# Performance work log

Hardware: AMD Instinct MI355X
Metric: run time of the kernel (lower is better)

## Reference

```python
import jax, jax.numpy as jnp
import numpy as np

B, T = 128, 50
VOCAB, EMB_D, GRU_H = 10000, 200, 100
HEADS, AHID, THID = 8, 96, 96

def _conv(x, w, b, pad):
    y = jax.lax.conv_general_dilated(x, w, (1, 1), pad,
        dimension_numbers=('NCHW', 'OIHW', 'NCHW'))
    return y + b[None, :, None, None]

def _bn(x, g, b, m, v):
    s = jax.lax.rsqrt(v + 1e-5)
    return (x - m[None, :, None, None]) * (g * s)[None, :, None, None] + b[None, :, None, None]

def _maxpool(x):
    return jax.lax.reduce_window(x, -jnp.inf, jax.lax.max, (1, 1, 2, 2), (1, 1, 2, 2), 'VALID')

def _resize(x):
    # F.interpolate(mode='bilinear', align_corners=False) == half-pixel bilinear, no antialias
    return jax.image.resize(x, (x.shape[0], x.shape[1], 25, 156), 'bilinear', antialias=False)

def _audio_attn(x, wq, bq, wk, bk, wv, bv):
    # x: [B,96,H,W]; wq: [heads,96,96] == stacked per-head 1x1 convs
    Q = jnp.einsum('bchw,noc->bnohw', x, wq) + bq[None, :, :, None, None]
    K = jnp.einsum('bchw,noc->bnohw', x, wk) + bk[None, :, :, None, None]
    V = jnp.einsum('bchw,noc->bnohw', x, wv) + bv[None, :, :, None, None]
    # torch F.softmax with no dim on a 4D tensor defaults to dim=1 (channels) -> axis=2 here
    return jax.nn.softmax(Q * K, axis=2) * V  # [B,heads,96,H,W]

def _text_attn(o, wq, bq, wk, bk, wv, bv):
    # o: [N,100]; wq: [heads,96,100] == stacked per-head Linear layers
    Q = jnp.einsum('nd,hod->nho', o, wq) + bq[None]
    K = jnp.einsum('nd,hod->nho', o, wk) + bk[None]
    V = jnp.einsum('nd,hod->nho', o, wv) + bv[None]
    a = jax.nn.softmax(Q * K, axis=2) * V  # 2D softmax default dim=1 -> over feature axis
    return a.reshape(o.shape[0], -1)  # head-concat order == torch cat along dim=1

def _gru(xs, w_ih, w_hh, b_ih, b_hh):
    # xs: [T,B,200]; torch gate order r, z, n; b_hn applied inside r-gating
    def step(h, x):
        gi = x @ w_ih.T + b_ih
        gh = h @ w_hh.T + b_hh
        ir, iz, inew = jnp.split(gi, 3, axis=1)
        hr, hz, hnew = jnp.split(gh, 3, axis=1)
        r = jax.nn.sigmoid(ir + hr)
        z = jax.nn.sigmoid(iz + hz)
        n = jnp.tanh(inew + r * hnew)
        h2 = (1.0 - z) * n + z * h
        return h2, h2
    h0 = jnp.zeros((xs.shape[1], GRU_H), xs.dtype)
    hT, outs = jax.lax.scan(step, h0, xs)
    return outs, hT

def _forward(tokens, lengths, mfcc_t, mfcc_f, mfcc_c, w1a, b1a, g1a, be1a, m1a, v1a, w1b, b1b, g1b, be1b, m1b, v1b, w2, b2, g2, be2, m2, v2, w3, b3, g3, be3, m3, v3, w4, b4, g4, be4, m4, v4, wq_a1, bq_a1, wk_a1, bk_a1, wv_a1, bv_a1, wq_a2, bq_a2, wk_a2, bk_a2, wv_a2, bv_a2, emb, w_ih, w_hh, b_ih, b_hh, wq_t1, bq_t1, wk_t1, bk_t1, wv_t1, bv_t1, wq_t2, bq_t2, wk_t2, bk_t2, wv_t2, bv_t2, w_fa, b_fa, w_ft, b_ft, w_e, b_e):
    # --- audio CNN stem (eval-mode batchnorm; dropout off) ---
    xa = jax.nn.relu(_bn(_conv(mfcc_t, w1a, b1a, 'VALID'), g1a, be1a, m1a, v1a))
    xb = jax.nn.relu(_bn(_conv(mfcc_f, w1b, b1b, 'VALID'), g1b, be1b, m1b, v1b))
    # NOTE: original source reuses conv1b/bn1b for the third input (faithful to that)
    xc = jax.nn.relu(_bn(_conv(mfcc_c, w1b, b1b, 'VALID'), g1b, be1b, m1b, v1b))
    x = jnp.concatenate([_resize(xa), _resize(xb), _resize(xc)], axis=1)  # [B,24,25,156]
    x = _maxpool(jax.nn.relu(_bn(_conv(x, w2, b2, [(1, 1), (1, 1)]), g2, be2, m2, v2)))  # [B,32,12,78]
    x = _maxpool(jax.nn.relu(_bn(_conv(x, w3, b3, [(1, 1), (1, 1)]), g3, be3, m3, v3)))  # [B,64,6,39]
    x = jax.nn.relu(_bn(_conv(x, w4, b4, [(1, 1), (1, 1)]), g4, be4, m4, v4))            # [B,96,6,39]
    # --- two stacked per-head audio attentions, then per-head spatial GAP ---
    a1 = _audio_attn(x, wq_a1, bq_a1, wk_a1, bk_a1, wv_a1, bv_a1).mean(axis=(-2, -1))  # [B,8,96]
    a2 = _audio_attn(x, wq_a2, bq_a2, wk_a2, bk_a2, wv_a2, bv_a2).mean(axis=(-2, -1))
    # forward() slices heads along the height concat and GAPs -> per head [stage1 96, stage2 96]
    self_attn_audio = jnp.concatenate([a1, a2], axis=2).reshape(x.shape[0], -1)  # [B,1536]
    # --- text branch: embedding + GRU (all lengths == T -> pack/pad is identity) ---
    ex = jnp.swapaxes(emb[tokens], 0, 1)  # [T,B,200]
    outs, h = _gru(ex, w_ih, w_hh, b_ih, b_hh)  # h: [B,100]
    output = jnp.swapaxes(outs, 0, 1).reshape(-1, GRU_H)  # [B*T,100]
    t1 = _text_attn(output, wq_t1, bq_t1, wk_t1, bk_t1, wv_t1, bv_t1)
    t2 = _text_attn(output, wq_t2, bq_t2, wk_t2, bk_t2, wv_t2, bv_t2)
    self_attn_text = jnp.concatenate([t1, t2], axis=1).reshape(x.shape[0], T, -1).sum(axis=1)  # [B,1536]
    # --- cross-modal gated fusion ---
    x_gap = x.mean(axis=(-2, -1))  # [B,96]
    a_text = jax.nn.softmax(x_gap @ w_fa.T + b_fa, axis=1)   # [B,100]
    attn_text_based_audio = a_text * h                        # [B,100]
    a_audio = jax.nn.softmax(h @ w_ft.T + b_ft, axis=1)      # [B,96]
    attn_audio_based_text = a_audio * x_gap                   # [B,96]
    feat = jnp.concatenate([self_attn_audio, self_attn_text,
                            attn_audio_based_text, attn_text_based_audio], axis=1)  # [B,3268]
    return feat @ w_e.T + b_e  # [B,4] emotion logits

def setup_inputs() -> dict:
    key = jax.random.key(0)
    ks = iter(jax.random.split(key, 100))
    nrm = lambda s, sc=0.05: jax.random.normal(next(ks), s, jnp.float32) * sc
    uni = lambda s: jax.random.uniform(next(ks), s, jnp.float32) * 0.5 + 0.5
    d = {}
    d['mfcc_t'] = jax.random.normal(next(ks), (B, 1, 200, 40), jnp.float32)
    d['mfcc_f'] = jax.random.normal(next(ks), (B, 1, 200, 40), jnp.float32)
    d['mfcc_c'] = jax.random.normal(next(ks), (B, 1, 200, 40), jnp.float32)
    d['tokens'] = jax.random.randint(next(ks), (B, T), 0, VOCAB)
    d['lengths'] = jnp.full((B,), T, jnp.int32)
    def bnp(pre, c):
        d['g' + pre] = 1.0 + nrm((c,)); d['be' + pre] = nrm((c,))
        d['m' + pre] = nrm((c,)); d['v' + pre] = uni((c,))
    d['w1a'] = nrm((8, 1, 5, 2), 0.2); d['b1a'] = nrm((8,)); bnp('1a', 8)
    d['w1b'] = nrm((8, 1, 2, 6), 0.2); d['b1b'] = nrm((8,)); bnp('1b', 8)
    d['w2'] = nrm((32, 24, 3, 3), 0.1); d['b2'] = nrm((32,)); bnp('2', 32)
    d['w3'] = nrm((64, 32, 3, 3), 0.1); d['b3'] = nrm((64,)); bnp('3', 64)
    d['w4'] = nrm((96, 64, 3, 3), 0.08); d['b4'] = nrm((96,)); bnp('4', 96)
    for s in ('1', '2'):
        for p in ('q', 'k', 'v'):
            d['w%s_a%s' % (p, s)] = nrm((HEADS, 96, 96), 0.1)
            d['b%s_a%s' % (p, s)] = nrm((HEADS, 96))
    d['emb'] = nrm((VOCAB, EMB_D), 0.1)
    d['w_ih'] = nrm((3 * GRU_H, EMB_D), 0.1); d['w_hh'] = nrm((3 * GRU_H, GRU_H), 0.1)
    d['b_ih'] = nrm((3 * GRU_H,)); d['b_hh'] = nrm((3 * GRU_H,))
    for s in ('1', '2'):
        for p in ('q', 'k', 'v'):
            d['w%s_t%s' % (p, s)] = nrm((HEADS, THID, GRU_H), 0.1)
            d['b%s_t%s' % (p, s)] = nrm((HEADS, THID))
    d['w_fa'] = nrm((100, 96), 0.1); d['b_fa'] = nrm((100,))
    d['w_ft'] = nrm((96, 100), 0.1); d['b_ft'] = nrm((96,))
    d['w_e'] = nrm((4, 2 * HEADS * AHID + 2 * HEADS * THID + 96 + 100), 0.05); d['b_e'] = nrm((4,))
    return d

def reference(mfcc_t, mfcc_f, mfcc_c, tokens, lengths, w1a, b1a, g1a, be1a, m1a, v1a, w1b, b1b, g1b, be1b, m1b, v1b, w2, b2, g2, be2, m2, v2, w3, b3, g3, be3, m3, v3, w4, b4, g4, be4, m4, v4, wq_a1, bq_a1, wk_a1, bk_a1, wv_a1, bv_a1, wq_a2, bq_a2, wk_a2, bk_a2, wv_a2, bv_a2, emb, w_ih, w_hh, b_ih, b_hh, wq_t1, bq_t1, wk_t1, bk_t1, wv_t1, bv_t1, wq_t2, bq_t2, wk_t2, bk_t2, wv_t2, bv_t2, w_fa, b_fa, w_ft, b_ft, w_e, b_e):
    return _forward(tokens, lengths, mfcc_t, mfcc_f, mfcc_c, w1a, b1a, g1a, be1a, m1a, v1a, w1b, b1b, g1b, be1b, m1b, v1b, w2, b2, g2, be2, m2, v2, w3, b3, g3, be3, m3, v3, w4, b4, g4, be4, m4, v4, wq_a1, bq_a1, wk_a1, bk_a1, wv_a1, bv_a1, wq_a2, bq_a2, wk_a2, bk_a2, wv_a2, bv_a2, emb, w_ih, w_hh, b_ih, b_hh, wq_t1, bq_t1, wk_t1, bk_t1, wv_t1, bv_t1, wq_t2, bq_t2, wk_t2, bk_t2, wv_t2, bv_t2, w_fa, b_fa, w_ft, b_ft, w_e, b_e)
```

## Files before the change

### kernel.cpp

```cpp
#include <hip/hip_runtime.h>
#include <math.h>

static constexpr int kB = 128;
static constexpr int kT = 50;

struct TDesc { const float* src; float* dst; int O; int C; int total; };
struct TPack { TDesc d[15]; };
__global__ void k_transpose_pack(TPack p, float* __restrict__ za) {
    if (blockIdx.y == 15) {
        for (int i = blockIdx.x * 256 + threadIdx.x; i < 196608; i += 76800)
            za[i] = 0.f;
        return;
    }
    TDesc t = p.d[blockIdx.y];
    int idx = blockIdx.x * 256 + threadIdx.x;
    if (idx >= t.total) return;
    int o = idx % t.O; int r = idx / t.O; int c = r % t.C; int n = r / t.C;
    t.dst[idx] = t.src[((size_t)n * t.O + o) * t.C + c];
}

__global__ void __launch_bounds__(320) k_gi(const int* __restrict__ tokens,
        const float* __restrict__ emb, const float* __restrict__ w_ih,
        const float* __restrict__ b_ih, float* __restrict__ GI) {
    int r0 = blockIdx.x * 8;
// ... 18 lines not shown
            }
        }
        #pragma unroll
        for (int r = 0; r < 8; ++r)
            GI[(size_t)(r0 + r) * 300 + tid] = acc[r];
    }
}

__global__ void __launch_bounds__(256) k_fat_stem_gru(
    const float* __restrict__ mt, const float* __restrict__ mf,
    const float* __restrict__ mc,
    const float* __restrict__ w1a, const float* __restrict__ b1a,
    const float* __restrict__ g1a, const float* __restrict__ be1a,
    const float* __restrict__ m1a, const float* __restrict__ v1a,
    const float* __restrict__ w1b, const float* __restrict__ b1b,
    const float* __restrict__ g1b, const float* __restrict__ be1b,
    const float* __restrict__ m1b, const float* __restrict__ v1b,
    float* __restrict__ out, int total,
    const float* __restrict__ GI, const float* __restrict__ w_hh,
    const float* __restrict__ b_hh, float* __restrict__ outsT) {
    if (blockIdx.x < 128) {
        const int b = blockIdx.x, tid = threadIdx.x;
        __shared__ float hs[100];
        __shared__ float gH[300];
        const float bias0 = b_hh[tid];
        const float bias1 = (tid < 44) ? b_hh[256 + tid] : 0.f;
        if (tid < 100) hs[tid] = 0.f;
        __syncthreads();
        for (int t = 0; t < kT; ++t) {
            {
                float gh = bias0;
                const float* wr = w_hh + (size_t)tid * 100;
                #pragma unroll
                for (int k4 = 0; k4 < 25; ++k4) {
                    float4 w4 = *(const float4*)(wr + k4 * 4);
                    float4 h4 = *(const float4*)&hs[k4 * 4];
                    gh += w4.x * h4.x + w4.y * h4.y + w4.z * h4.z + w4.w * h4.w;
                }
                gH[tid] = gh;
            }
            if (tid < 44) {
                float gh = bias1;
                const float* wr = w_hh + (size_t)(256 + tid) * 100;
                #pragma unroll
                for (int k4 = 0; k4 < 25; ++k4) {
                    float4 w4 = *(const float4*)(wr + k4 * 4);
                    float4 h4 = *(const float4*)&hs[k4 * 4];
                    gh += w4.x * h4.x + w4.y * h4.y + w4.z * h4.z + w4.w * h4.w;
                }
                gH[256 + tid] = gh;
            }
            __syncthreads();
            if (tid < 100) {
                const float* gi = GI + ((size_t)b * kT + t) * 300;
                float r = 1.f / (1.f + expf(-(gi[tid] + gH[tid])));
                float z = 1.f / (1.f + expf(-(gi[100 + tid] + gH[100 + tid])));
                float nn = tanhf(gi[200 + tid] + r * gH[200 + tid]);
                float h2 = (1.f - z) * nn + z * hs[tid];
                hs[tid] = h2;
                outsT[((size_t)b * 100 + tid) * kT + t] = h2;
            }
            __syncthreads();
        }
        return;
    }
    int idx = (blockIdx.x - 128) * 256 + threadIdx.x;
    if (idx >= total) return;
    int ox = idx % 156; int t = idx / 156;
    int oy = t % 25; t /= 25;
    int grp = t % 3; int b = t / 3;
    const float* src; int Hc, Wc;
    const float *wb0, *cb, *g, *be, *m, *v;
    if (grp == 0) { src = mt; Hc = 196; Wc = 39; wb0 = w1a;
                    cb = b1a; g = g1a; be = be1a; m = m1a; v = v1a; }
    else          { src = (grp == 1 ? mf : mc); Hc = 199; Wc = 35; wb0 = w1b;
                    cb = b1b; g = g1b; be = be1b; m = m1b; v = v1b; }
    float sy = (oy + 0.5f) * ((float)Hc / 25.f) - 0.5f;
    float sx = (ox + 0.5f) * ((float)Wc / 156.f) - 0.5f;
    float fy0 = floorf(sy), fx0 = floorf(sx);
    float fy = sy - fy0, fx = sx - fx0;
    int y0 = (int)fy0, x0 = (int)fx0;
    int y0c = min(max(y0, 0), Hc - 1), y1c = min(max(y0 + 1, 0), Hc - 1);
    int x0c = min(max(x0, 0), Wc - 1), x1c = min(max(x0 + 1, 0), Wc - 1);
    bool xs = (x1c == x0c), ys = (y1c == y0c);
    const float* p = src + (size_t)b * 8000;
    float* ob_ = out + (((size_t)b * 24 + grp * 8) * 25 + oy) * 156 + ox;
    const float w00 = (1.f - fy) * (1.f - fx), w01 = (1.f - fy) * fx;
    const float w10 = fy * (1.f - fx),         w11 = fy * fx;
    if (grp == 0) {
        float W[6][3];
        #pragma unroll
        for (int r = 0; r < 6; ++r) {
            int rr = min(y0c + r, 199);
            #pragma unroll
            for (int cc = 0; cc < 3; ++cc)
                W[r][cc] = p[rr * 40 + min(x0c + cc, 39)];
        }
        #pragma unroll
        for (int c = 0; c < 8; ++c) {
            const float* wb = wb0 + c * 10;
            float a00 = 0.f, a01 = 0.f, a10 = 0.f, a11 = 0.f;
            #pragma unroll
            for (int ky = 0; ky < 5; ++ky)
                #pragma unroll
                for (int kx = 0; kx < 2; ++kx) {
                    float wv = wb[ky * 2 + kx];
                    a00 += W[ky][kx] * wv;     a01 += W[ky][kx + 1] * wv;
                    a10 += W[ky + 1][kx] * wv; a11 += W[ky + 1][kx + 1] * wv;
                }
            float t00 = a00;
            float t01 = xs ? a00 : a01;
            float t10 = ys ? a00 : a10;
            float t11 = xs ? (ys ? a00 : a10) : (ys ? a01 : a11);
            float s = g[c] * rsqrtf(v[c] + 1e-5f);
            float bias = (cb[c] - m[c]) * s + be[c];
            float r00 = fmaxf(t00 * s + bias, 0.f), r01 = fmaxf(t01 * s + bias, 0.f);
            float r10 = fmaxf(t10 * s + bias, 0.f), r11 = fmaxf(t11 * s + bias, 0.f);
            ob_[c * 3900] = r00 * w00 + r01 * w01 + r10 * w10 + r11 * w11;
        }
    } else {
        float W[3][7];
        #pragma unroll
        for (int r = 0; r < 3; ++r) {
            int rr = min(y0c + r, 199);
            #pragma unroll
            for (int cc = 0; cc < 7; ++cc)
                W[r][cc] = p[rr * 40 + min(x0c + cc, 39)];
        }
        #pragma unroll
        for (int c = 0; c < 8; ++c) {
            const float* wb = wb0 + c * 12;
            float a00 = 0.f, a01 = 0.f, a10 = 0.f, a11 = 0.f;
            #pragma unroll
            for (int ky = 0; ky < 2; ++ky)
                #pragma unroll
                for (int kx = 0; kx < 6; ++kx) {
                    float wv = wb[ky * 6 + kx];
                    a00 += W[ky][kx] * wv;     a01 += W[ky][kx + 1] * wv;
                    a10 += W[ky + 1][kx] * wv; a11 += W[ky + 1][kx + 1] * wv;
                }
            float t00 = a00;
            float t01 = xs ? a00 : a01;
            float t10 = ys ? a00 : a10;
            float t11 = xs ? (ys ? a00 : a10) : (ys ? a01 : a11);
            float s = g[c] * rsqrtf(v[c] + 1e-5f);
            float bias = (cb[c] - m[c]) * s + be[c];
            float r00 = fmaxf(t00 * s + bias, 0.f), r01 = fmaxf(t01 * s + bias, 0.f);
            float r10 = fmaxf(t10 * s + bias, 0.f), r11 = fmaxf(t11 * s + bias, 0.f);
            ob_[c * 3900] = r00 * w00 + r01 * w01 + r10 * w10 + r11 * w11;
        }
    }
}

template<int CIN, int CI_T, int H, int W, int ROWS, int NPX, bool POOL>
__global__ void __launch_bounds__(256) k_conv16(
    const float* __restrict__ in, const float* __restrict__ wT,
    const float* __restrict__ cb, const float* __restrict__ g,
    const float* __restrict__ be, const float* __restrict__ m,
    const float* __restrict__ v, float* __restrict__ out, int COUT, int PHT) {
    constexpr int WP = W + 2;
    constexpr int RP = ROWS + 2;
    constexpr int STAGE = CI_T * RP * WP;
    __shared__ float sx[STAGE];
    __shared__ float sw[CI_T * 9 * 16];
    const int b = blockIdx.x, rt = blockIdx.y, oc0 = blockIdx.z * 16;
    const int row0 = rt * ROWS;
    const int tid = threadIdx.x;

    int off[NPX]; bool val[NPX];
    #pragma unroll
    for (int j = 0; j < NPX; ++j) {
        int px = tid + j * 256;
        int oy = px / W, ox = px - oy * W;
        bool ok = (px < ROWS * W) && (row0 + oy < H);
        val[j] = ok;
        off[j] = ok ? (oy * WP + ox) : 0;
    }

    float acc[NPX][16];
    #pragma unroll
    for (int j = 0; j < NPX; ++j)
        #pragma unroll
        for (int o = 0; o < 16; ++o) acc[j][o] = 0.f;

    for (int c0 = 0; c0 < CIN; c0 += CI_T) {
        __syncthreads();
        for (int e = tid; e < STAGE; e += 256) {
            int ci = e / (RP * WP);
            int rem = e - ci * RP * WP;
            int r = rem / WP;
            int xx = rem - r * WP;
            int iy = row0 - 1 + r;
            int ix = xx - 1;
            float vv = 0.f;
            if (iy >= 0 && iy < H && ix >= 0 && ix < W)
                vv = in[((size_t)(b * CIN + c0 + ci) * H + iy) * W + ix];
            sx[e] = vv;
        }
        for (int e = tid; e < CI_T * 9 * 16; e += 256) {
            int rk = e >> 4;
            int o = e & 15;
            sw[e] = wT[((size_t)c0 * 9 + rk) * COUT + oc0 + o];
        }
        __syncthreads();
        #pragma unroll 1
        for (int cl = 0; cl < CI_T; ++cl) {
            const float* sxc = sx + cl * RP * WP;
            #pragma unroll
            for (int k = 0; k < 9; ++k) {
                const int ky = k / 3, kx = k % 3;
                const float* wb_ = sw + (cl * 9 + k) * 16;
                const float4 wa = *(const float4*)(wb_);
                const float4 wb2 = *(const float4*)(wb_ + 4);
                const float4 wc = *(const float4*)(wb_ + 8);
                const float4 wd = *(const float4*)(wb_ + 12);
                #pragma unroll
                for (int j = 0; j < NPX; ++j) {
                    float xv = sxc[off[j] + ky * WP + kx];
                    acc[j][0]  += xv * wa.x;  acc[j][1]  += xv * wa.y;
                    acc[j][2]  += xv * wa.z;  acc[j][3]  += xv * wa.w;
                    acc[j][4]  += xv * wb2.x; acc[j][5]  += xv * wb2.y;
                    acc[j][6]  += xv * wb2.z; acc[j][7]  += xv * wb2.w;
                    acc[j][8]  += xv * wc.x;  acc[j][9]  += xv * wc.y;
                    acc[j][10] += xv * wc.z;  acc[j][11] += xv * wc.w;
                    acc[j][12] += xv * wd.x;  acc[j][13] += xv * wd.y;
                    acc[j][14] += xv * wd.z;  acc[j][15] += xv * wd.w;
                }
            }
        }
    }
    float sc[16], bi[16];
    #pragma unroll
    for (int o = 0; o < 16; ++o) {
        float s = g[oc0 + o] * rsqrtf(v[oc0 + o] + 1e-5f);
        sc[o] = s; bi[o] = (cb[oc0 + o] - m[oc0 + o]) * s + be[oc0 + o];
    }
    if (!POOL) {
        #pragma unroll
        for (int j = 0; j < NPX; ++j) if (val[j]) {
            int px = tid + j * 256;
            int oy = row0 + px / W, ox = px % W;
            #pragma unroll
            for (int o = 0; o < 16; ++o)
                out[((size_t)(b * COUT + oc0 + o) * H + oy) * W + ox] =
                    fmaxf(acc[j][o] * sc[o] + bi[o], 0.f);
        }
    } else {
        constexpr int PH = ROWS / 2, PW = W / 2, PT = PH * PW;
        const int prow0 = rt * PH;
        for (int o = 0; o < 16; ++o) {
            __syncthreads();
            #pragma unroll
            for (int j = 0; j < NPX; ++j) if (val[j]) {
                int px = tid + j * 256;
                sx[px] = fmaxf(acc[j][o] * sc[o] + bi[o], 0.f);
            }
            __syncthreads();
            for (int e = tid; e < PT; e += 256) {
                int py = e / PW, pxl = e - py * PW;
                const float* r0 = sx + (2 * py) * W + 2 * pxl;
                float mv = fmaxf(fmaxf(r0[0], r0[1]), fmaxf(r0[W], r0[W + 1]));
                out[((size_t)(b * COUT + oc0 + o) * PHT + prow0 + py) * PW + pxl] = mv;
            }
        }
    }
}

__global__ void __launch_bounds__(256, 2) k_fat_attn(
    const float* __restrict__ x,
    const float* __restrict__ wq1, const float* __restrict__ bq1,
    const float* __restrict__ wk1, const float* __restrict__ bk1,
    const float* __restrict__ wv1, const float* __restrict__ bv1,
    const float* __restrict__ wq2, const float* __restrict__ bq2,
    const float* __restrict__ wk2, const float* __restrict__ bk2,
    const float* __restrict__ wv2, const float* __restrict__ bv2,
    float* __restrict__ afeat,
    const float* __restrict__ outsT,
    const float* __restrict__ wqt1, const float* __restrict__ bqt1,
    const float* __restrict__ wkt1, const float* __restrict__ bkt1,
    const float* __restrict__ wvt1, const float* __restrict__ bvt1,
    const float* __restrict__ wqt2, const float* __restrict__ bqt2,
    const float* __restrict__ wkt2, const float* __restrict__ bkt2,
    const float* __restrict__ wvt2, const float* __restrict__ bvt2,
    float* __restrict__ tfeat, float* __restrict__ xgap) {
    __shared__ float smem[7040];
    const int bx = blockIdx.x;
    const int tid = threadIdx.x;

    if (bx >= 6144) {
        int b = bx - 6144;
        int wave = tid >> 6, lane = tid & 63;
        for (int c = wave; c < 96; c += 4) {
            const float* row = x + ((size_t)b * 96 + c) * 234;
            float s = 0.f;
            for (int p = lane; p < 234; p += 64) s += row[p];
            #pragma unroll
            for (int off = 1; off < 64; off <<= 1) s += __shfl_xor(s, off);
            if (lane == 0) xgap[b * 96 + c] = s * (1.f / 234.f);
        }
        return;
    }
    if (bx >= 4096) {
        int a = bx - 4096;
        const int b = a & 127;
        int rem = a >> 7;
        const int stage = rem & 1, n = rem >> 1;
        const float* wq = (stage ? wqt2 : wqt1) + n * 9600;
        const float* wk = (stage ? wkt2 : wkt1) + n * 9600;
        const float* wv = (stage ? wvt2 : wvt1) + n * 9600;
        const float* bqn = (stage ? bqt2 : bqt1) + n * 96;
        const float* bkn = (stage ? bkt2 : bkt1) + n * 96;
        const float* bvn = (stage ? bvt2 : bvt1) + n * 96;
        const int to = tid >> 4, tpg = tid & 15;
        const int ob = to * 6;
        const int tA = tpg * 4;
        float* sxc = smem;
        float* sw = smem + 1280;
        float* sred = sw;
        const float* xb = outsT + (size_t)b * (100 * kT);

        float qa[6][4], ka[6][4], va[6][4];
        #pragma unroll
        for (int j = 0; j < 6; ++j) {
            float bq_ = bqn[ob + j], bk_ = bkn[ob + j], bv_ = bvn[ob + j];
            #pragma unroll
            for (int i = 0; i < 4; ++i) { qa[j][i] = bq_; ka[j][i] = bk_; va[j][i] = bv_; }
        }
        for (int c0 = 0; c0 < 100; c0 += 20) {
            __syncthreads();
            for (int e = tid; e < 1280; e += 256) {
                int r = e >> 6, tt = e & 63;
                sxc[e] = (tt < kT) ? xb[(c0 + r) * kT + tt] : 0.f;
            }
            for (int e4 = tid; e4 < 1440; e4 += 256) {
                int mat = (e4 >= 960) ? 2 : (e4 >= 480 ? 1 : 0);
                int r4 = e4 - mat * 480;
                const float* wsrc = (mat == 0) ? wq : (mat == 1 ? wk : wv);
                *(float4*)(sw + mat * 1920 + r4 * 4) = *(const float4*)(wsrc + c0 * 96 + r4 * 4);
            }
            __syncthreads();
            #pragma unroll 4
            for (int cc = 0; cc < 20; ++cc) {
                float4 xa = *(const float4*)(sxc + cc * 64 + tA);
                const float* wr = sw + cc * 96 + ob;
                float2 q01 = *(const float2*)(wr);
                float2 q23 = *(const float2*)(wr + 2);
                float2 q45 = *(const float2*)(wr + 4);
                float2 k01 = *(const float2*)(wr + 1920);
                float2 k23 = *(const float2*)(wr + 1922);
                float2 k45 = *(const float2*)(wr + 1924);
                float2 v01 = *(const float2*)(wr + 3840);
                float2 v23 = *(const float2*)(wr + 3842);
                float2 v45 = *(const float2*)(wr + 3844);
                float wqv[6] = {q01.x, q01.y, q23.x, q23.y, q45.x, q45.y};
                float wkv[6] = {k01.x, k01.y, k23.x, k23.y, k45.x, k45.y};
                float wvv[6] = {v01.x, v01.y, v23.x, v23.y, v45.x, v45.y};
                #pragma unroll
                for (int j = 0; j < 6; ++j) {
                    qa[j][0] += wqv[j] * xa.x; qa[j][1] += wqv[j] * xa.y;
                    qa[j][2] += wqv[j] * xa.z; qa[j][3] += wqv[j] * xa.w;
                    ka[j][0] += wkv[j] * xa.x; ka[j][1] += wkv[j] * xa.y;
                    ka[j][2] += wkv[j] * xa.z; ka[j][3] += wkv[j] * xa.w;
                    va[j][0] += wvv[j] * xa.x; va[j][1] += wvv[j] * xa.y;
                    va[j][2] += wvv[j] * xa.z; va[j][3] += wvv[j] * xa.w;
                }
            }
        }
        float pmx[4] = {-1e30f, -1e30f, -1e30f, -1e30f};
        #pragma unroll
        for (int j = 0; j < 6; ++j)
            #pragma unroll
            for (int i = 0; i < 4; ++i) {
                float sv = qa[j][i] * ka[j][i];
                qa[j][i] = sv;
                pmx[i] = fmaxf(pmx[i], sv);
            }
        __syncthreads();
        #pragma unroll
        for (int i = 0; i < 4; ++i) sred[to * 64 + tA + i] = pmx[i];
        __syncthreads();
        float m_[4];
        #pragma unroll
        for (int i = 0; i < 4; ++i) {
            float mm = -1e30f;
            for (int t = 0; t < 16; ++t) mm = fmaxf(mm, sred[t * 64 + tA + i]);
            m_[i] = mm;
        }
        __syncthreads();
        float z[4] = {0.f, 0.f, 0.f, 0.f};
        #pragma unroll
        for (int j = 0; j < 6; ++j)
            #pragma unroll
            for (int i = 0; i < 4; ++i) {
                float e = __expf(qa[j][i] - m_[i]);
                qa[j][i] = e;
                z[i] += e;
            }
        #pragma unroll
        for (int i = 0; i < 4; ++i) sred[to * 64 + tA + i] = z[i];
        __syncthreads();
        float rz[4];
        #pragma unroll
        for (int i = 0; i < 4; ++i) {
            float zs = 0.f;
            for (int t = 0; t < 16; ++t) zs += sred[t * 64 + tA + i];
            rz[i] = (tA + i < kT) ? 1.f / zs : 0.f;
        }
        __syncthreads();
        #pragma unroll
        for (int j = 0; j < 6; ++j) {
            float po = qa[j][0] * rz[0] * va[j][0]
                     + qa[j][1] * rz[1] * va[j][1]
                     + qa[j][2] * rz[2] * va[j][2]
                     + qa[j][3] * rz[3] * va[j][3];
            sred[(ob + j) * 16 + tpg] = po;
        }
        __syncthreads();
        if (tid < 96) {
            float ssum = 0.f;
            #pragma unroll
            for (int t = 0; t < 16; ++t) ssum += sred[tid * 16 + t];
            tfeat[b * 1536 + stage * 768 + n * 96 + tid] = ssum;
        }
        return;
    }

    const int a = bx;
    const int xp = a & 255;
    const int b = xp >> 1, pt = xp & 1;
    const int n = (a >> 8) & 7, stage = a >> 11;
    const float* wq = (stage ? wq2 : wq1) + n * 9216;
    const float* wk = (stage ? wk2 : wk1) + n * 9216;
    const float* wv = (stage ? wv2 : wv1) + n * 9216;
    const float* bqn = (stage ? bq2 : bq1) + n * 96;
    const float* bkn = (stage ? bk2 : bk1) + n * 96;
    const float* bvn = (stage ? bv2 : bv1) + n * 96;
    const int to = tid >> 4, tpg = tid & 15;
    const int ob = to * 6;
    const int pA = tpg * 4;
    const int p0 = pt * 128;

    float* sxc = smem;
    float* sw = smem + 2048;
    float* sred = sw;

    const float* xb = x + (size_t)b * (96 * 234) + p0;

    float qa[6][8], ka[6][8], va[6][8];
    #pragma unroll
    for (int j = 0; j < 6; ++j) {
        float bq_ = bqn[ob + j], bk_ = bkn[ob + j], bv_ = bvn[ob + j];
        #pragma unroll
        for (int i = 0; i < 8; ++i) { qa[j][i] = bq_; ka[j][i] = bk_; va[j][i] = bv_; }
    }

    for (int c0 = 0; c0 < 96; c0 += 16) {
        __syncthreads();
        {
            #pragma unroll
            for (int it = 0; it < 4; ++it) {
                int e2 = tid + it * 256;
                int r = e2 >> 6, c2 = (e2 & 63) * 2;
                float2 v = make_float2(0.f, 0.f);
                if (p0 + c2 < 234) v = *(const float2*)(xb + (c0 + r) * 234 + c2);
                *(float2*)(sxc + r * 128 + c2) = v;
            }
        }
        for (int e4 = tid; e4 < 1152; e4 += 256) {
            int mat = (e4 >= 768) ? 2 : (e4 >= 384 ? 1 : 0);
            int r4 = e4 - mat * 384;
            const float* wsrc = (mat == 0) ? wq : (mat == 1 ? wk : wv);
            *(float4*)(sw + mat * 1536 + r4 * 4) = *(const float4*)(wsrc + c0 * 96 + r4 * 4);
        }
        __syncthreads();
        #pragma unroll 2
        for (int cc = 0; cc < 16; ++cc) {
            float4 xa = *(const float4*)(sxc + cc * 128 + pA);
            float4 xc = *(const float4*)(sxc + cc * 128 + 64 + pA);
            const float* wr = sw + cc * 96 + ob;
            float2 q01 = *(const float2*)(wr);
            float2 q23 = *(const float2*)(wr + 2);
            float2 q45 = *(const float2*)(wr + 4);
            float2 k01 = *(const float2*)(wr + 1536);
            float2 k23 = *(const float2*)(wr + 1538);
            float2 k45 = *(const float2*)(wr + 1540);
            float2 v01 = *(const float2*)(wr + 3072);
            float2 v23 = *(const float2*)(wr + 3074);
            float2 v45 = *(const float2*)(wr + 3076);
            float wqv[6] = {q01.x, q01.y, q23.x, q23.y, q45.x, q45.y};
            float wkv[6] = {k01.x, k01.y, k23.x, k23.y, k45.x, k45.y};
            float wvv[6] = {v01.x, v01.y, v23.x, v23.y, v45.x, v45.y};
            #pragma unroll
            for (int j = 0; j < 6; ++j) {
                qa[j][0] += wqv[j] * xa.x; qa[j][1] += wqv[j] * xa.y;
                qa[j][2] += wqv[j] * xa.z; qa[j][3] += wqv[j] * xa.w;
                qa[j][4] += wqv[j] * xc.x; qa[j][5] += wqv[j] * xc.y;
                qa[j][6] += wqv[j] * xc.z; qa[j][7] += wqv[j] * xc.w;
                ka[j][0] += wkv[j] * xa.x; ka[j][1] += wkv[j] * xa.y;
                ka[j][2] += wkv[j] * xa.z; ka[j][3] += wkv[j] * xa.w;
                ka[j][4] += wkv[j] * xc.x; ka[j][5] += wkv[j] * xc.y;
                ka[j][6] += wkv[j] * xc.z; ka[j][7] += wkv[j] * xc.w;
                va[j][0] += wvv[j] * xa.x; va[j][1] += wvv[j] * xa.y;
                va[j][2] += wvv[j] * xa.z; va[j][3] += wvv[j] * xa.w;
                va[j][4] += wvv[j] * xc.x; va[j][5] += wvv[j] * xc.y;
                va[j][6] += wvv[j] * xc.z; va[j][7] += wvv[j] * xc.w;
            }
        }
    }

    int col[8];
    #pragma unroll
    for (int i = 0; i < 4; ++i) { col[i] = pA + i; col[4 + i] = 64 + pA + i; }

    float pmx[8];
    #pragma unroll
    for (int i = 0; i < 8; ++i) pmx[i] = -1e30f;
    #pragma unroll
    for (int j = 0; j < 6; ++j)
        #pragma unroll
        for (int i = 0; i < 8; ++i) {
            float sv = qa[j][i] * ka[j][i];
            qa[j][i] = sv;
            pmx[i] = fmaxf(pmx[i], sv);
        }
    __syncthreads();
    #pragma unroll
    for (int i = 0; i < 8; ++i) sred[to * 128 + col[i]] = pmx[i];
    __syncthreads();
    float m_[8];
    #pragma unroll
    for (int i = 0; i < 8; ++i) {
        float mm = -1e30f;
        for (int t = 0; t < 16; ++t) mm = fmaxf(mm, sred[t * 128 + col[i]]);
        m_[i] = mm;
    }
    __syncthreads();
    float z[8];
    #pragma unroll
    for (int i = 0; i < 8; ++i) z[i] = 0.f;
    #pragma unroll
    for (int j = 0; j < 6; ++j)
        #pragma unroll
        for (int i = 0; i < 8; ++i) {
            float e = __expf(qa[j][i] - m_[i]);
            qa[j][i] = e;
            z[i] += e;
        }
    #pragma unroll
    for (int i = 0; i < 8; ++i) sred[to * 128 + col[i]] = z[i];
    __syncthreads();
    float rz[8];
    #pragma unroll
    for (int i = 0; i < 8; ++i) {
        float zs = 0.f;
        for (int t = 0; t < 16; ++t) zs += sred[t * 128 + col[i]];
        rz[i] = (p0 + col[i] < 234) ? 1.f / zs : 0.f;
    }
    __syncthreads();
    #pragma unroll
    for (int j = 0; j < 6; ++j) {
        float po = 0.f;
        #pragma unroll
        for (int i = 0; i < 8; ++i) po += qa[j][i] * rz[i] * va[j][i];
        sred[(ob + j) * 16 + tpg] = po;
    }
    __syncthreads();
    if (tid < 96) {
        float ssum = 0.f;
        #pragma unroll
        for (int t = 0; t < 16; ++t) ssum += sred[tid * 16 + t];
        atomicAdd(afeat + b * 1536 + n * 192 + stage * 96 + tid, ssum * (1.f / 234.f));
    }
}

__global__ void __launch_bounds__(128) k_final(const float* __restrict__ xgap,
    const float* __restrict__ outsT, const float* __restrict__ afeat,
    const float* __restrict__ tfeat,
    const float* __restrict__ w_fa, const float* __restrict__ b_fa,
    const float* __restrict__ w_ft, const float* __restrict__ b_ft,
    const float* __restrict__ w_e, const float* __restrict__ b_e,
    float* __restrict__ out) {
    int b = blockIdx.x; int tid = threadIdx.x;
    __shared__ float xg[96], hv[100], st[100], sa[96], aat[96], atba[100];
    __shared__ float redm[2], reds[2];
    if (tid < 96) xg[tid] = xgap[b * 96 + tid];
    if (tid < 100) hv[tid] = outsT[((size_t)b * 100 + tid) * kT + (kT - 1)];
    __syncthreads();
    if (tid < 100) {
        float acc = b_fa[tid];
        const float* wr = w_fa + tid * 96;
        for (int c = 0; c < 96; ++c) acc += wr[c] * xg[c];
        st[tid] = acc;
    }
    if (tid < 96) {
        float acc = b_ft[tid];
        const float* wr = w_ft + tid * 100;
        for (int c = 0; c < 100; ++c) acc += wr[c] * hv[c];
        sa[tid] = acc;
    }
    __syncthreads();
    if (tid == 0) {
        float mxv = -1e30f; for (int i = 0; i < 100; ++i) mxv = fmaxf(mxv, st[i]);
        float s = 0.f; for (int i = 0; i < 100; ++i) s += expf(st[i] - mxv);
        redm[0] = mxv; reds[0] = s;
    }
    if (tid == 1) {
        float mxv = -1e30f; for (int i = 0; i < 96; ++i) mxv = fmaxf(mxv, sa[i]);
        float s = 0.f; for (int i = 0; i < 96; ++i) s += expf(sa[i] - mxv);
        redm[1] = mxv; reds[1] = s;
    }
    __syncthreads();
    if (tid < 100) atba[tid] = expf(st[tid] - redm[0]) / reds[0] * hv[tid];
    if (tid < 96)  aat[tid]  = expf(sa[tid] - redm[1]) / reds[1] * xg[tid];
    __syncthreads();
    float a0 = 0.f, a1 = 0.f, a2 = 0.f, a3 = 0.f;
    for (int col = tid; col < 3268; col += 128) {
        float f;
        if (col < 1536)      f = afeat[b * 1536 + col];
        else if (col < 3072) f = tfeat[b * 1536 + col - 1536];
        else if (col < 3168) f = aat[col - 3072];
        else                 f = atba[col - 3168];
        a0 += w_e[col] * f;            a1 += w_e[3268 + col] * f;
        a2 += w_e[2 * 3268 + col] * f; a3 += w_e[3 * 3268 + col] * f;
    }
    __shared__ float r4[4][128];
    r4[0][tid] = a0; r4[1][tid] = a1; r4[2][tid] = a2; r4[3][tid] = a3;
    __syncthreads();
    if (tid < 4) {
        float s = 0.f;
        for (int i = 0; i < 128; ++i) s += r4[tid][i];
        out[b * 4 + tid] = s + b_e[tid];
    }
}

extern "C" void kernel_launch(void* const* d_in, const int* in_sizes, int n_in,
                              void* d_out, int out_size, void* d_ws, size_t ws_size,
                              hipStream_t stream) {
    (void)in_sizes; (void)n_in; (void)out_size; (void)ws_size;
    const float* mfcc_t = (const float*)d_in[0];
    const float* mfcc_f = (const float*)d_in[1];
    const float* mfcc_c = (const float*)d_in[2];
    const int*   tokens = (const int*)d_in[3];
    const float *w1a = (const float*)d_in[5],  *b1a = (const float*)d_in[6],
                *g1a = (const float*)d_in[7],  *be1a = (const float*)d_in[8],
                *m1a = (const float*)d_in[9],  *v1a = (const float*)d_in[10];
    const float *w1b = (const float*)d_in[11], *b1b = (const float*)d_in[12],
                *g1b = (const float*)d_in[13], *be1b = (const float*)d_in[14],
                *m1b = (const float*)d_in[15], *v1b = (const float*)d_in[16];
    const float *w2 = (const float*)d_in[17], *b2 = (const float*)d_in[18],
                *g2 = (const float*)d_in[19], *be2 = (const float*)d_in[20],
                *m2 = (const float*)d_in[21], *v2 = (const float*)d_in[22];
    const float *w3 = (const float*)d_in[23], *b3 = (const float*)d_in[24],
                *g3 = (const float*)d_in[25], *be3 = (const float*)d_in[26],
                *m3 = (const float*)d_in[27], *v3 = (const float*)d_in[28];
    const float *w4 = (const float*)d_in[29], *b4 = (const float*)d_in[30],
                *g4 = (const float*)d_in[31], *be4 = (const float*)d_in[32],
                *m4 = (const float*)d_in[33], *v4 = (const float*)d_in[34];
    const float *wq_a1 = (const float*)d_in[35], *bq_a1 = (const float*)d_in[36],
                *wk_a1 = (const float*)d_in[37], *bk_a1 = (const float*)d_in[38],
                *wv_a1 = (const float*)d_in[39], *bv_a1 = (const float*)d_in[40];
    const float *wq_a2 = (const float*)d_in[41], *bq_a2 = (const float*)d_in[42],
                *wk_a2 = (const float*)d_in[43], *bk_a2 = (const float*)d_in[44],
                *wv_a2 = (const float*)d_in[45], *bv_a2 = (const float*)d_in[46];
    const float *emb  = (const float*)d_in[47];
    const float *w_ih = (const float*)d_in[48], *w_hh = (const float*)d_in[49],
                *b_ih = (const float*)d_in[50], *b_hh = (const float*)d_in[51];
    const float *wq_t1 = (const float*)d_in[52], *bq_t1 = (const float*)d_in[53],
                *wk_t1 = (const float*)d_in[54], *bk_t1 = (const float*)d_in[55],
                *wv_t1 = (const float*)d_in[56], *bv_t1 = (const float*)d_in[57];
    const float *wq_t2 = (const float*)d_in[58], *bq_t2 = (const float*)d_in[59],
                *wk_t2 = (const float*)d_in[60], *bk_t2 = (const float*)d_in[61],
                *wv_t2 = (const float*)d_in[62], *bv_t2 = (const float*)d_in[63];
    const float *w_fa = (const float*)d_in[64], *b_fa = (const float*)d_in[65],
                *w_ft = (const float*)d_in[66], *b_ft = (const float*)d_in[67],
                *w_e  = (const float*)d_in[68], *b_e  = (const float*)d_in[69];

    float* ws = (float*)d_ws;
    const size_t Z0 = 0;
    const size_t Z1 = 22091776ull;
    const size_t OUTS  = 34072576ull;
    const size_t AFEAT = 34712576ull;
    const size_t TFEAT = 34909184ull;
    const size_t XGAP  = 35105792ull;
    const size_t WT    = 35118080ull;
    float* GI = ws + Z0;
    float* X1 = ws + Z1;
    float* P2 = ws + Z0;
    float* P3 = ws + Z1;
    float* X4 = ws + Z0;
    float* outsT = ws + OUTS;
    float* afeat = ws + AFEAT;
    float* tfeat = ws + TFEAT;
    float* xgap  = ws + XGAP;
    float* wqa1t = ws + WT;
    float* wka1t = wqa1t + 73728; float* wva1t = wka1t + 73728;
    float* wqa2t = wva1t + 73728; float* wka2t = wqa2t + 73728; float* wva2t = wka2t + 73728;
    float* wqt1t = wva2t + 73728;
    float* wkt1t = wqt1t + 76800; float* wvt1t = wkt1t + 76800;
    float* wqt2t = wvt1t + 76800; float* wkt2t = wqt2t + 76800; float* wvt2t = wkt2t + 76800;
    float* wT2 = tfeat;
    float* wT3 = tfeat + 6912;
    float* wT4 = tfeat + 25344;

    TPack tp;
    tp.d[0]  = {wq_a1, wqa1t, 96, 96, 73728};
    tp.d[1]  = {wk_a1, wka1t, 96, 96, 73728};
    tp.d[2]  = {wv_a1, wva1t, 96, 96, 73728};
    tp.d[3]  = {wq_a2, wqa2t, 96, 96, 73728};
    tp.d[4]  = {wk_a2, wka2t, 96, 96, 73728};
    tp.d[5]  = {wv_a2, wva2t, 96, 96, 73728};
    tp.d[6]  = {w2, wT2, 32, 216, 6912};
    tp.d[7]  = {w3, wT3, 64, 288, 18432};
    tp.d[8]  = {w4, wT4, 96, 576, 55296};
    tp.d[9]  = {wq_t1, wqt1t, 96, 100, 76800};
    tp.d[10] = {wk_t1, wkt1t, 96, 100, 76800};
    tp.d[11] = {wv_t1, wvt1t, 96, 100, 76800};
    tp.d[12] = {wq_t2, wqt2t, 96, 100, 76800};
    tp.d[13] = {wk_t2, wkt2t, 96, 100, 76800};
    tp.d[14] = {wv_t2, wvt2t, 96, 100, 76800};
    k_transpose_pack<<<dim3(300, 16), 256, 0, stream>>>(tp, afeat);

    k_gi<<<kB * kT / 8, 320, 0, stream>>>(tokens, emb, w_ih, b_ih, GI);

    k_fat_stem_gru<<<5978, 256, 0, stream>>>(mfcc_t, mfcc_f, mfcc_c,
        w1a, b1a, g1a, be1a, m1a, v1a,
        w1b, b1b, g1b, be1b, m1b, v1b, X1, 1497600,
        GI, w_hh, b_hh, outsT);

    k_conv16<24, 8, 25, 156, 8, 5, true><<<dim3(128, 3, 2), 256, 0, stream>>>(
        X1, wT2, b2, g2, be2, m2, v2, P2, 32, 12);
    k_conv16<32, 8, 12, 78, 12, 4, true><<<dim3(128, 1, 4), 256, 0, stream>>>(
        P2, wT3, b3, g3, be3, m3, v3, P3, 64, 6);
    k_conv16<64, 16, 6, 39, 6, 1, false><<<dim3(128, 1, 6), 256, 0, stream>>>(
        P3, wT4, b4, g4, be4, m4, v4, X4, 96, 0);

    k_fat_attn<<<6272, 256, 0, stream>>>(X4,
        wqa1t, bq_a1, wka1t, bk_a1, wva1t, bv_a1,
        wqa2t, bq_a2, wka2t, bk_a2, wva2t, bv_a2, afeat,
        outsT,
        wqt1t, bq_t1, wkt1t, bk_t1, wvt1t, bv_t1,
        wqt2t, bq_t2, wkt2t, bk_t2, wvt2t, bv_t2, tfeat, xgap);

    k_final<<<kB, 128, 0, stream>>>(xgap, outsT, afeat, tfeat,
                                    w_fa, b_fa, w_ft, b_ft, w_e, b_e, (float*)d_out);
}
```

Before: 1.281 ms.

## Co-schedule text attention blocks alongside conv2/conv3/conv4 launches

Moves the 2048 text-attention blocks out of the big attention kernel and distributes them across the three conv kernels (1024, 512, 512 extra blocks). Text attention depends only on the GRU output, so it can fill idle CUs while the small conv grids run. The conv weight transposes are moved to a separate workspace region so they no longer alias tfeat, which is now written during the conv stage. The risk is extra shared memory per fused kernel and uneven block mixes hurting occupancy.

```diff
diff --git a/kernel.cpp b/kernel.cpp
--- a/kernel.cpp
+++ b/kernel.cpp
@@ -194,8 +194,140 @@
     }
 }
 
-template<int CIN, int CI_T, int H, int W, int ROWS, int NPX, bool POOL>
-__global__ void __launch_bounds__(256) k_conv16(
+__device__ __forceinline__ void text_attn_block(int a, float* smem,
+    const float* __restrict__ outsT,
+    const float* __restrict__ wqt1, const float* __restrict__ bqt1,
+    const float* __restrict__ wkt1, const float* __restrict__ bkt1,
+    const float* __restrict__ wvt1, const float* __restrict__ bvt1,
+    const float* __restrict__ wqt2, const float* __restrict__ bqt2,
+    const float* __restrict__ wkt2, const float* __restrict__ bkt2,
+    const float* __restrict__ wvt2, const float* __restrict__ bvt2,
+    float* __restrict__ tfeat) {
+    const int tid = threadIdx.x;
+    const int b = a & 127;
+    int rem = a >> 7;
+    const int stage = rem & 1, n = rem >> 1;
+    const float* wq = (stage ? wqt2 : wqt1) + n * 9600;
+    const float* wk = (stage ? wkt2 : wkt1) + n * 9600;
+    const float* wv = (stage ? wvt2 : wvt1) + n * 9600;
+    const float* bqn = (stage ? bqt2 : bqt1) + n * 96;
+    const float* bkn = (stage ? bkt2 : bkt1) + n * 96;
+    const float* bvn = (stage ? bvt2 : bvt1) + n * 96;
+    const int to = tid >> 4, tpg = tid & 15;
+    const int ob = to * 6;
+    const int tA = tpg * 4;
+    float* sxc = smem;
+    float* sw = smem + 1280;
+    float* sred = sw;
+    const float* xb = outsT + (size_t)b * (100 * kT);
+
+    float qa[6][4], ka[6][4], va[6][4];
+    #pragma unroll
+    for (int j = 0; j < 6; ++j) {
+        float bq_ = bqn[ob + j], bk_ = bkn[ob + j], bv_ = bvn[ob + j];
+        #pragma unroll
+        for (int i = 0; i < 4; ++i) { qa[j][i] = bq_; ka[j][i] = bk_; va[j][i] = bv_; }
+    }
+    for (int c0 = 0; c0 < 100; c0 += 20) {
+        __syncthreads();
+        for (int e = tid; e < 1280; e += 256) {
+            int r = e >> 6, tt = e & 63;
+            sxc[e] = (tt < kT) ? xb[(c0 + r) * kT + tt] : 0.f;
+        }
+        for (int e4 = tid; e4 < 1440; e4 += 256) {
+            int mat = (e4 >= 960) ? 2 : (e4 >= 480 ? 1 : 0);
+            int r4 = e4 - mat * 480;
+            const float* wsrc = (mat == 0) ? wq : (mat == 1 ? wk : wv);
+            *(float4*)(sw + mat * 1920 + r4 * 4) = *(const float4*)(wsrc + c0 * 96 + r4 * 4);
+        }
+        __syncthreads();
+        #pragma unroll 4
+        for (int cc = 0; cc < 20; ++cc) {
+            float4 xa = *(const float4*)(sxc + cc * 64 + tA);
+            const float* wr = sw + cc * 96 + ob;
+            float2 q01 = *(const float2*)(wr);
+            float2 q23 = *(const float2*)(wr + 2);
+            float2 q45 = *(const float2*)(wr + 4);
+            float2 k01 = *(const float2*)(wr + 1920);
+            float2 k23 = *(const float2*)(wr + 1922);
+            float2 k45 = *(const float2*)(wr + 1924);
+            float2 v01 = *(const float2*)(wr + 3840);
+            float2 v23 = *(const float2*)(wr + 3842);
+            float2 v45 = *(const float2*)(wr + 3844);
+            float wqv[6] = {q01.x, q01.y, q23.x, q23.y, q45.x, q45.y};
+            float wkv[6] = {k01.x, k01.y, k23.x, k23.y, k45.x, k45.y};
+            float wvv[6] = {v01.x, v01.y, v23.x, v23.y, v45.x, v45.y};
+            #pragma unroll
+            for (int j = 0; j < 6; ++j) {
+                qa[j][0] += wqv[j] * xa.x; qa[j][1] += wqv[j] * xa.y;
+                qa[j][2] += wqv[j] * xa.z; qa[j][3] += wqv[j] * xa.w;
+                ka[j][0] += wkv[j] * xa.x; ka[j][1] += wkv[j] * xa.y;
+                ka[j][2] += wkv[j] * xa.z; ka[j][3] += wkv[j] * xa.w;
+                va[j][0] += wvv[j] * xa.x; va[j][1] += wvv[j] * xa.y;
+                va[j][2] += wvv[j] * xa.z; va[j][3] += wvv[j] * xa.w;
+            }
+        }
+    }
+    float pmx[4] = {-1e30f, -1e30f, -1e30f, -1e30f};
+    #pragma unroll
+    for (int j = 0; j < 6; ++j)
+        #pragma unroll
+        for (int i = 0; i < 4; ++i) {
+            float sv = qa[j][i] * ka[j][i];
+            qa[j][i] = sv;
+            pmx[i] = fmaxf(pmx[i], sv);
+        }
+    __syncthreads();
+    #pragma unroll
+    for (int i = 0; i < 4; ++i) sred[to * 64 + tA + i] = pmx[i];
+    __syncthreads();
+    float m_[4];
+    #pragma unroll
+    for (int i = 0; i < 4; ++i) {
+        float mm = -1e30f;
+        for (int t = 0; t < 16; ++t) mm = fmaxf(mm, sred[t * 64 + tA + i]);
+        m_[i] = mm;
+    }
+    __syncthreads();
+    float z[4] = {0.f, 0.f, 0.f, 0.f};
+    #pragma unroll
+    for (int j = 0; j < 6; ++j)
+        #pragma unroll
+        for (int i = 0; i < 4; ++i) {
+            float e = __expf(qa[j][i] - m_[i]);
+            qa[j][i] = e;
+            z[i] += e;
+        }
+    #pragma unroll
+    for (int i = 0; i < 4; ++i) sred[to * 64 + tA + i] = z[i];
+    __syncthreads();
+    float rz[4];
+    #pragma unroll
+    for (int i = 0; i < 4; ++i) {
+        float zs = 0.f;
+        for (int t = 0; t < 16; ++t) zs += sred[t * 64 + tA + i];
+        rz[i] = (tA + i < kT) ? 1.f / zs : 0.f;
+    }
+    __syncthreads();
+    #pragma unroll
+    for (int j = 0; j < 6; ++j) {
+        float po = qa[j][0] * rz[0] * va[j][0]
+                 + qa[j][1] * rz[1] * va[j][1]
+                 + qa[j][2] * rz[2] * va[j][2]
+                 + qa[j][3] * rz[3] * va[j][3];
+        sred[(ob + j) * 16 + tpg] = po;
+    }
+    __syncthreads();
+    if (tid < 96) {
+        float ssum = 0.f;
+        #pragma unroll
+        for (int t = 0; t < 16; ++t) ssum += sred[tid * 16 + t];
+        tfeat[b * 1536 + stage * 768 + n * 96 + tid] = ssum;
+    }
+}
+
+template<int CIN, int CI_T, int H, int W, int ROWS, int NPX, bool POOL, int NRT>
+__device__ __forceinline__ void conv16_body(int bxl, float* smem,
     const float* __restrict__ in, const float* __restrict__ wT,
     const float* __restrict__ cb, const float* __restrict__ g,
     const float* __restrict__ be, const float* __restrict__ m,
@@ -203,9 +335,11 @@
     constexpr int WP = W + 2;
     constexpr int RP = ROWS + 2;
     constexpr int STAGE = CI_T * RP * WP;
-    __shared__ float sx[STAGE];
-    __shared__ float sw[CI_T * 9 * 16];
-    const int b = blockIdx.x, rt = blockIdx.y, oc0 = blockIdx.z * 16;
+    float* sx = smem;
+    float* sw = smem + STAGE;
+    const int b = bxl & 127;
+    const int rem = bxl >> 7;
+    const int rt = rem % NRT, oc0 = (rem / NRT) * 16;
     const int row0 = rt * ROWS;
     const int tid = threadIdx.x;
 
@@ -229,9 +363,9 @@
         __syncthreads();
         for (int e = tid; e < STAGE; e += 256) {
             int ci = e / (RP * WP);
-            int rem = e - ci * RP * WP;
-            int r = rem / WP;
-            int xx = rem - r * WP;
+            int rem2 = e - ci * RP * WP;
+            int r = rem2 / WP;
+            int xx = rem2 - r * WP;
             int iy = row0 - 1 + r;
             int ix = xx - 1;
             float vv = 0.f;
@@ -308,7 +442,79 @@
     }
 }
 
-__global__ void __launch_bounds__(256, 2) k_fat_attn(
+__global__ void __launch_bounds__(256) k_fat_conv2_text(
+    const float* __restrict__ in, const float* __restrict__ wT,
+    const float* __restrict__ cb, const float* __restrict__ g,
+    const float* __restrict__ be, const float* __restrict__ m,
+    const float* __restrict__ v, float* __restrict__ out,
+    const float* __restrict__ outsT,
+    const float* __restrict__ wqt1, const float* __restrict__ bqt1,
+    const float* __restrict__ wkt1, const float* __restrict__ bkt1,
+    const float* __restrict__ wvt1, const float* __restrict__ bvt1,
+    const float* __restrict__ wqt2, const float* __restrict__ bqt2,
+    const float* __restrict__ wkt2, const float* __restrict__ bkt2,
+    const float* __restrict__ wvt2, const float* __restrict__ bvt2,
+    float* __restrict__ tfeat, int txtBase) {
+    __shared__ float smem[13792];
+    if (blockIdx.x < 768) {
+        conv16_body<24, 8, 25, 156, 8, 5, true, 3>(blockIdx.x, smem,
+            in, wT, cb, g, be, m, v, out, 32, 12);
+        return;
+    }
+    text_attn_block((blockIdx.x - 768) + txtBase, smem, outsT,
+        wqt1, bqt1, wkt1, bkt1, wvt1, bvt1,
+        wqt2, bqt2, wkt2, bkt2, wvt2, bvt2, tfeat);
+}
+
+__global__ void __launch_bounds__(256) k_fat_conv3_text(
+    const float* __restrict__ in, const float* __restrict__ wT,
+    const float* __restrict__ cb, const float* __restrict__ g,
+    const float* __restrict__ be, const float* __restrict__ m,
+    const float* __restrict__ v, float* __restrict__ out,
+    const float* __restrict__ outsT,
+    const float* __restrict__ wqt1, const float* __restrict__ bqt1,
+    const float* __restrict__ wkt1, const float* __restrict__ bkt1,
+    const float* __restrict__ wvt1, const float* __restrict__ bvt1,
+    const float* __restrict__ wqt2, const float* __restrict__ bqt2,
+    const float* __restrict__ wkt2, const float* __restrict__ bkt2,
+    const float* __restrict__ wvt2, const float* __restrict__ bvt2,
+    float* __restrict__ tfeat, int txtBase) {
+    __shared__ float smem[10112];
+    if (blockIdx.x < 512) {
+        conv16_body<32, 8, 12, 78, 12, 4, true, 1>(blockIdx.x, smem,
+            in, wT, cb, g, be, m, v, out, 64, 6);
+        return;
+    }
+    text_attn_block((blockIdx.x - 512) + txtBase, smem, outsT,
+        wqt1, bqt1, wkt1, bkt1, wvt1, bvt1,
+        wqt2, bqt2, wkt2, bkt2, wvt2, bvt2, tfeat);
+}
+
+__global__ void __launch_bounds__(256) k_fat_conv4_text(
+    const float* __restrict__ in, const float* __restrict__ wT,
+    const float* __restrict__ cb, const float* __restrict__ g,
+    const float* __restrict__ be, const float* __restrict__ m,
+    const float* __restrict__ v, float* __restrict__ out,
+    const float* __restrict__ outsT,
+    const float* __restrict__ wqt1, const float* __restrict__ bqt1,
+    const float* __restrict__ wkt1, const float* __restrict__ bkt1,
+    const float* __restrict__ wvt1, const float* __restrict__ bvt1,
+    const float* __restrict__ wqt2, const float* __restrict__ bqt2,
+    const float* __restrict__ wkt2, const float* __restrict__ bkt2,
+    const float* __restrict__ wvt2, const float* __restrict__ bvt2,
+    float* __restrict__ tfeat, int txtBase) {
+    __shared__ float smem[7552];
+    if (blockIdx.x < 768) {
+        conv16_body<64, 16, 6, 39, 6, 1, false, 1>(blockIdx.x, smem,
+            in, wT, cb, g, be, m, v, out, 96, 0);
+        return;
+    }
+    text_attn_block((blockIdx.x - 768) + txtBase, smem, outsT,
+        wqt1, bqt1, wkt1, bkt1, wvt1, bvt1,
+        wqt2, bqt2, wkt2, bkt2, wvt2, bvt2, tfeat);
+}
+
+__global__ void __launch_bounds__(256, 2) k_fat_audio(
     const float* __restrict__ x,
     const float* __restrict__ wq1, const float* __restrict__ bq1,
     const float* __restrict__ wk1, const float* __restrict__ bk1,
@@ -316,21 +522,13 @@
     const float* __restrict__ wq2, const float* __restrict__ bq2,
     const float* __restrict__ wk2, const float* __restrict__ bk2,
     const float* __restrict__ wv2, const float* __restrict__ bv2,
-    float* __restrict__ afeat,
-    const float* __restrict__ outsT,
-    const float* __restrict__ wqt1, const float* __restrict__ bqt1,
-    const float* __restrict__ wkt1, const float* __restrict__ bkt1,
-    const float* __restrict__ wvt1, const float* __restrict__ bvt1,
-    const float* __restrict__ wqt2, const float* __restrict__ bqt2,
-    const float* __restrict__ wkt2, const float* __restrict__ bkt2,
-    const float* __restrict__ wvt2, const float* __restrict__ bvt2,
-    float* __restrict__ tfeat, float* __restrict__ xgap) {
-    __shared__ float smem[7040];
+    float* __restrict__ afeat, float* __restrict__ xgap) {
+    __shared__ float smem[6656];
     const int bx = blockIdx.x;
     const int tid = threadIdx.x;
 
-    if (bx >= 6144) {
-        int b = bx - 6144;
+    if (bx >= 4096) {
+        int b = bx - 4096;
         int wave = tid >> 6, lane = tid & 63;
         for (int c = wave; c < 96; c += 4) {
             const float* row = x + ((size_t)b * 96 + c) * 234;
@@ -339,130 +537,6 @@
             #pragma unroll
             for (int off = 1; off < 64; off <<= 1) s += __shfl_xor(s, off);
             if (lane == 0) xgap[b * 96 + c] = s * (1.f / 234.f);
-        }
-        return;
-    }
-    if (bx >= 4096) {
-        int a = bx - 4096;
-        const int b = a & 127;
-        int rem = a >> 7;
-        const int stage = rem & 1, n = rem >> 1;
-        const float* wq = (stage ? wqt2 : wqt1) + n * 9600;
-        const float* wk = (stage ? wkt2 : wkt1) + n * 9600;
-        const float* wv = (stage ? wvt2 : wvt1) + n * 9600;
-        const float* bqn = (stage ? bqt2 : bqt1) + n * 96;
-        const float* bkn = (stage ? bkt2 : bkt1) + n * 96;
-        const float* bvn = (stage ? bvt2 : bvt1) + n * 96;
-        const int to = tid >> 4, tpg = tid & 15;
-        const int ob = to * 6;
-        const int tA = tpg * 4;
-        float* sxc = smem;
-        float* sw = smem + 1280;
-        float* sred = sw;
-        const float* xb = outsT + (size_t)b * (100 * kT);
-
-        float qa[6][4], ka[6][4], va[6][4];
-        #pragma unroll
-        for (int j = 0; j < 6; ++j) {
-            float bq_ = bqn[ob + j], bk_ = bkn[ob + j], bv_ = bvn[ob + j];
-            #pragma unroll
-            for (int i = 0; i < 4; ++i) { qa[j][i] = bq_; ka[j][i] = bk_; va[j][i] = bv_; }
-        }
-        for (int c0 = 0; c0 < 100; c0 += 20) {
-            __syncthreads();
-            for (int e = tid; e < 1280; e += 256) {
-                int r = e >> 6, tt = e & 63;
-                sxc[e] = (tt < kT) ? xb[(c0 + r) * kT + tt] : 0.f;
-            }
-            for (int e4 = tid; e4 < 1440; e4 += 256) {
-                int mat = (e4 >= 960) ? 2 : (e4 >= 480 ? 1 : 0);
-                int r4 = e4 - mat * 480;
-                const float* wsrc = (mat == 0) ? wq : (mat == 1 ? wk : wv);
-                *(float4*)(sw + mat * 1920 + r4 * 4) = *(const float4*)(wsrc + c0 * 96 + r4 * 4);
-            }
-            __syncthreads();
-            #pragma unroll 4
-            for (int cc = 0; cc < 20; ++cc) {
-                float4 xa = *(const float4*)(sxc + cc * 64 + tA);
-                const float* wr = sw + cc * 96 + ob;
-                float2 q01 = *(const float2*)(wr);
-                float2 q23 = *(const float2*)(wr + 2);
-                float2 q45 = *(const float2*)(wr + 4);
-                float2 k01 = *(const float2*)(wr + 1920);
-                float2 k23 = *(const float2*)(wr + 1922);
-                float2 k45 = *(const float2*)(wr + 1924);
-                float2 v01 = *(const float2*)(wr + 3840);
-                float2 v23 = *(const float2*)(wr + 3842);
-                float2 v45 = *(const float2*)(wr + 3844);
-                float wqv[6] = {q01.x, q01.y, q23.x, q23.y, q45.x, q45.y};
-                float wkv[6] = {k01.x, k01.y, k23.x, k23.y, k45.x, k45.y};
-                float wvv[6] = {v01.x, v01.y, v23.x, v23.y, v45.x, v45.y};
-                #pragma unroll
-                for (int j = 0; j < 6; ++j) {
-                    qa[j][0] += wqv[j] * xa.x; qa[j][1] += wqv[j] * xa.y;
-                    qa[j][2] += wqv[j] * xa.z; qa[j][3] += wqv[j] * xa.w;
-                    ka[j][0] += wkv[j] * xa.x; ka[j][1] += wkv[j] * xa.y;
-                    ka[j][2] += wkv[j] * xa.z; ka[j][3] += wkv[j] * xa.w;
-                    va[j][0] += wvv[j] * xa.x; va[j][1] += wvv[j] * xa.y;
-                    va[j][2] += wvv[j] * xa.z; va[j][3] += wvv[j] * xa.w;
-                }
-            }
-        }
-        float pmx[4] = {-1e30f, -1e30f, -1e30f, -1e30f};
-        #pragma unroll
-        for (int j = 0; j < 6; ++j)
-            #pragma unroll
-            for (int i = 0; i < 4; ++i) {
-                float sv = qa[j][i] * ka[j][i];
-                qa[j][i] = sv;
-                pmx[i] = fmaxf(pmx[i], sv);
-            }
-        __syncthreads();
-        #pragma unroll
-        for (int i = 0; i < 4; ++i) sred[to * 64 + tA + i] = pmx[i];
-        __syncthreads();
-        float m_[4];
-        #pragma unroll
-        for (int i = 0; i < 4; ++i) {
-            float mm = -1e30f;
-            for (int t = 0; t < 16; ++t) mm = fmaxf(mm, sred[t * 64 + tA + i]);
-            m_[i] = mm;
-        }
-        __syncthreads();
-        float z[4] = {0.f, 0.f, 0.f, 0.f};
-        #pragma unroll
-        for (int j = 0; j < 6; ++j)
-            #pragma unroll
-            for (int i = 0; i < 4; ++i) {
-                float e = __expf(qa[j][i] - m_[i]);
-                qa[j][i] = e;
-                z[i] += e;
-            }
-        #pragma unroll
-        for (int i = 0; i < 4; ++i) sred[to * 64 + tA + i] = z[i];
-        __syncthreads();
-        float rz[4];
-        #pragma unroll
-        for (int i = 0; i < 4; ++i) {
-            float zs = 0.f;
-            for (int t = 0; t < 16; ++t) zs += sred[t * 64 + tA + i];
-            rz[i] = (tA + i < kT) ? 1.f / zs : 0.f;
-        }
-        __syncthreads();
-        #pragma unroll
-        for (int j = 0; j < 6; ++j) {
-            float po = qa[j][0] * rz[0] * va[j][0]
-                     + qa[j][1] * rz[1] * va[j][1]
-                     + qa[j][2] * rz[2] * va[j][2]
-                     + qa[j][3] * rz[3] * va[j][3];
-            sred[(ob + j) * 16 + tpg] = po;
-        }
-        __syncthreads();
-        if (tid < 96) {
-            float ssum = 0.f;
-            #pragma unroll
-            for (int t = 0; t < 16; ++t) ssum += sred[tid * 16 + t];
-            tfeat[b * 1536 + stage * 768 + n * 96 + tid] = ssum;
         }
         return;
     }
@@ -740,9 +814,9 @@
     float* wqt1t = wva2t + 73728;
     float* wkt1t = wqt1t + 76800; float* wvt1t = wkt1t + 76800;
     float* wqt2t = wvt1t + 76800; float* wkt2t = wqt2t + 76800; float* wvt2t = wkt2t + 76800;
-    float* wT2 = tfeat;
-    float* wT3 = tfeat + 6912;
-    float* wT4 = tfeat + 25344;
+    float* wT2 = ws + 4000000;
+    float* wT3 = wT2 + 6912;
+    float* wT4 = wT3 + 18432;
 
     TPack tp;
     tp.d[0]  = {wq_a1, wqa1t, 96, 96, 73728};
@@ -769,19 +843,22 @@
         w1b, b1b, g1b, be1b, m1b, v1b, X1, 1497600,
         GI, w_hh, b_hh, outsT);
 
-    k_conv16<24, 8, 25, 156, 8, 5, true><<<dim3(128, 3, 2), 256, 0, stream>>>(
-        X1, wT2, b2, g2, be2, m2, v2, P2, 32, 12);
-    k_conv16<32, 8, 12, 78, 12, 4, true><<<dim3(128, 1, 4), 256, 0, stream>>>(
-        P2, wT3, b3, g3, be3, m3, v3, P3, 64, 6);
-    k_conv16<64, 16, 6, 39, 6, 1, false><<<dim3(128, 1, 6), 256, 0, stream>>>(
-        P3, wT4, b4, g4, be4, m4, v4, X4, 96, 0);
-
-    k_fat_attn<<<6272, 256, 0, stream>>>(X4,
+    k_fat_conv2_text<<<1792, 256, 0, stream>>>(
+        X1, wT2, b2, g2, be2, m2, v2, P2,
+        outsT, wqt1t, bq_t1, wkt1t, bk_t1, wvt1t, bv_t1,
+        wqt2t, bq_t2, wkt2t, bk_t2, wvt2t, bv_t2, tfeat, 0);
+    k_fat_conv3_text<<<1024, 256, 0, stream>>>(
+        P2, wT3, b3, g3, be3, m3, v3, P3,
+        outsT, wqt1t, bq_t1, wkt1t, bk_t1, wvt1t, bv_t1,
+        wqt2t, bq_t2, wkt2t, bk_t2, wvt2t, bv_t2, tfeat, 1024);
+    k_fat_conv4_text<<<1280, 256, 0, stream>>>(
+        P3, wT4, b4, g4, be4, m4, v4, X4,
+        outsT, wqt1t, bq_t1, wkt1t, bk_t1, wvt1t, bv_t1,
+        wqt2t, bq_t2, wkt2t, bk_t2, wvt2t, bv_t2, tfeat, 1536);
+
+    k_fat_audio<<<4224, 256, 0, stream>>>(X4,
         wqa1t, bq_a1, wka1t, bk_a1, wva1t, bv_a1,
-        wqa2t, bq_a2, wka2t, bk_a2, wva2t, bv_a2, afeat,
-        outsT,
-        wqt1t, bq_t1, wkt1t, bk_t1, wvt1t, bv_t1,
-        wqt2t, bq_t2, wkt2t, bk_t2, wvt2t, bv_t2, tfeat, xgap);
+        wqa2t, bq_a2, wka2t, bk_a2, wva2t, bv_a2, afeat, xgap);
 
     k_final<<<kB, 128, 0, stream>>>(xgap, outsT, afeat, tfeat,
                                     w_fa, b_fa, w_ft, b_ft, w_e, b_e, (float*)d_out);
```

Result: no change. 1.298 ms (+1.3%).
